# Performance work log

Hardware: AMD Instinct MI355X
Metric: run time of the kernel (lower is better)

The kernel has to match this reference:

```python
import jax, jax.numpy as jnp
import numpy as np

T, N, F_IN, H, HEADS, R, E, L, C = 8, 20000, 128, 128, 4, 12, 40000, 2, 16
D = H // HEADS


def setup_inputs() -> dict:
    key = jax.random.key(0)
    ks = jax.random.split(key, 24)
    s = 0.05  # weight scale to keep activations well-conditioned
    return {
        "x": jax.random.normal(ks[0], (T, N, F_IN), jnp.float32),
        "edge_src": jax.random.randint(ks[1], (R, E), 0, N),
        "edge_dst": jax.random.randint(ks[2], (R, E), 0, N),
        "rel_src_type": jax.random.randint(ks[3], (R,), 0, T),
        "rel_dst_type": jax.random.randint(ks[4], (R,), 0, T),
        "Wenc": jax.random.normal(ks[5], (T, F_IN, H)) * s,
        "benc": jax.random.normal(ks[6], (T, H)) * s,
        "Wk": jax.random.normal(ks[7], (L, T, H, H)) * s,
        "bk": jax.random.normal(ks[8], (L, T, H)) * s,
        "Wq": jax.random.normal(ks[9], (L, T, H, H)) * s,
        "bq": jax.random.normal(ks[10], (L, T, H)) * s,
        "Wv": jax.random.normal(ks[11], (L, T, H, H)) * s,
        "bv": jax.random.normal(ks[12], (L, T, H)) * s,
        "Wa": jax.random.normal(ks[13], (L, T, H, H)) * s,
        "ba": jax.random.normal(ks[14], (L, T, H)) * s,
        "skip": jax.random.normal(ks[15], (L, T)),
        "a_rel": jax.random.normal(ks[16], (L, R, HEADS, D, D)) * s,
        "m_rel": jax.random.normal(ks[17], (L, R, HEADS, D, D)) * s,
        "p_rel": jnp.ones((L, R, HEADS), jnp.float32),
        "Wout": jax.random.normal(ks[18], (H, C)) * s,
        "bout": jax.random.normal(ks[19], (C,)) * s,
    }


def _hgt_layer(x, Wk, bk, Wq, bq, Wv, bv, Wa, ba, skip, a_rel, m_rel, p_rel,
               edge_src, edge_dst, src_t, dst_t):
    # x: [T, N, H]; per-type k/q/v projections
    k = (jnp.einsum('tnh,thg->tng', x, Wk) + bk[:, None, :]).reshape(T, N, HEADS, D)
    q = (jnp.einsum('tnh,thg->tng', x, Wq) + bq[:, None, :]).reshape(T, N, HEADS, D)
    v = (jnp.einsum('tnh,thg->tng', x, Wv) + bv[:, None, :]).reshape(T, N, HEADS, D)

    # per-relation transforms on the (smaller) node side, then gather per edge
    k_rel = jnp.einsum('rnhd,rhde->rnhe', k[src_t], a_rel)  # [R, N, HEADS, D]
    v_rel = jnp.einsum('rnhd,rhde->rnhe', v[src_t], m_rel)
    gsrc = edge_src[:, :, None, None]
    gdst = edge_dst[:, :, None, None]
    k_e = jnp.take_along_axis(k_rel, gsrc, axis=1)          # [R, E, HEADS, D]
    v_e = jnp.take_along_axis(v_rel, gsrc, axis=1)
    q_e = jnp.take_along_axis(q[dst_t], gdst, axis=1)

    score = (q_e * k_e).sum(-1) * p_rel[:, None, :] / np.sqrt(D)  # [R, E, HEADS]

    # softmax per (edge-type, destination node): segment id = r*N + dst
    seg = (jnp.arange(R)[:, None] * N + edge_dst).reshape(-1)     # [R*E]
    sc = score.reshape(R * E, HEADS)
    m = jax.lax.stop_gradient(jax.ops.segment_max(sc, seg, num_segments=R * N))
    a = jnp.exp(sc - m[seg])
    denom = jax.ops.segment_sum(a, seg, num_segments=R * N)
    alpha = a / denom[seg]                                        # [R*E, HEADS]

    msg = (v_e.reshape(R * E, HEADS, D) * alpha[:, :, None]).reshape(R * E, H)
    # group='sum' across relations into (dst_type, dst_node)
    agg_seg = (dst_t[:, None] * N + edge_dst).reshape(-1)
    agg = jax.ops.segment_sum(msg, agg_seg, num_segments=T * N).reshape(T, N, H)

    out = jnp.einsum('tnh,thg->tng', jax.nn.gelu(agg, approximate=False), Wa) + ba[:, None, :]
    beta = jax.nn.sigmoid(skip)[:, None, None]
    return beta * out + (1.0 - beta) * x


def reference(x, edge_src, edge_dst, rel_src_type, rel_dst_type, Wenc, benc,
              Wk, bk, Wq, bq, Wv, bv, Wa, ba, skip, a_rel, m_rel, p_rel,
              Wout, bout):
    # per-node-type Linear + ReLU encode
    h = jax.nn.relu(jnp.einsum('tnf,tfh->tnh', x, Wenc) + benc[:, None, :])
    for l in range(L):
        h = _hgt_layer(h, Wk[l], bk[l], Wq[l], bq[l], Wv[l], bv[l], Wa[l], ba[l],
                       skip[l], a_rel[l], m_rel[l], p_rel[l],
                       edge_src, edge_dst, rel_src_type, rel_dst_type)
    # final Linear on the 'book' node type (index 0)
    return h[0] @ Wout + bout
```

## Files before the change

### kernel.cpp

```cpp
#include <hip/hip_runtime.h>
#include <cstdint>
#include <cstddef>

#define TT 8
#define NN 20000
#define FIN 128
#define HH 128
#define NHEADS 4
#define DD 32
#define RR 12
#define EE 40000
#define LL 2
#define CC 16
#define RN (RR*NN)
#define RE (RR*EE)
#define TNH ((size_t)TT*NN*HH)

struct Job { const float* in; const float* w; const float* b; float* out; };
struct Jobs8  { Job j[8]; };
struct Jobs16 { Job j[16]; };

__global__ __launch_bounds__(256) void zero_kernel(float4* __restrict__ p, int n4) {
    int i = blockIdx.x * 256 + threadIdx.x;
    int stride = gridDim.x * 256;
    for (; i < n4; i += stride) p[i] = make_float4(0.f, 0.f, 0.f, 0.f);
}

__global__ __launch_bounds__(256) void hist_kernel(const int* __restrict__ edge_dst,
                                                   int* __restrict__ cnt) {
    int g = blockIdx.x * 256 + threadIdx.x;
    if (g < RE) {
        int r = g / EE;
        atomicAdd(&cnt[r * NN + edge_dst[g]], 1);
    }
}

__global__ __launch_bounds__(256) void scan_local(const int* __restrict__ in,
                                                  int* __restrict__ out,
                                                  int* __restrict__ bsum, int n) {
    __shared__ int sh[256];
    int t = threadIdx.x;
    int base = blockIdx.x * 1024 + t * 4;
    int v0 = (base + 0 < n) ? in[base + 0] : 0;
    int v1 = (base + 1 < n) ? in[base + 1] : 0;
    int v2 = (base + 2 < n) ? in[base + 2] : 0;
    int v3 = (base + 3 < n) ? in[base + 3] : 0;
    int s = v0 + v1 + v2 + v3;
    sh[t] = s;
    __syncthreads();
    for (int off = 1; off < 256; off <<= 1) {
        int tmp = (t >= off) ? sh[t - off] : 0;
        __syncthreads();
        sh[t] += tmp;
        __syncthreads();
    }
    int incl = sh[t];
    int e = incl - s;
    if (t == 255) bsum[blockIdx.x] = incl;
    if (base + 0 < n) out[base + 0] = e; e += v0;
    if (base + 1 < n) out[base + 1] = e; e += v1;
    if (base + 2 < n) out[base + 2] = e; e += v2;
    if (base + 3 < n) out[base + 3] = e;
}

__global__ __launch_bounds__(256) void scan_bsum(int* __restrict__ bsum, int nb) {
    __shared__ int sh[256];
    int t = threadIdx.x;
    int v = (t < nb) ? bsum[t] : 0;
    sh[t] = v;
    __syncthreads();
    for (int off = 1; off < 256; off <<= 1) {
        int tmp = (t >= off) ? sh[t - off] : 0;
        __syncthreads();
        sh[t] += tmp;
        __syncthreads();
    }
    if (t < nb) bsum[t] = sh[t] - v;
}

__global__ __launch_bounds__(256) void scan_add(int* __restrict__ ofs,
                                                int* __restrict__ cursor,
                                                const int* __restrict__ bsum, int n) {
    int i = blockIdx.x * 256 + threadIdx.x;
    if (i < n) {
        int v = ofs[i] + bsum[i >> 10];
        ofs[i] = v;
        cursor[i] = v;
    }
}

__global__ __launch_bounds__(256) void scatter_kernel(const int* __restrict__ edge_dst,
                                                      int* __restrict__ cursor,
                                                      int* __restrict__ eidx) {
    int g = blockIdx.x * 256 + threadIdx.x;
    if (g < RE) {
        int r = g / EE;
        int pos = atomicAdd(&cursor[r * NN + edge_dst[g]], 1);
        eidx[pos] = g;
    }
}

template<int ACT, typename JT>
__global__ __launch_bounds__(256) void gemm128(const JT jt,
                                               const float* __restrict__ skip_l) {
    __shared__ float lw[32][128];
    __shared__ float li[32][132];
    const Job jb = jt.j[blockIdx.y];
    const int tid = threadIdx.x;
    const int row0 = blockIdx.x * 128;
    const int col = (tid & 31) * 4;
    const int rbase = (tid >> 5) * 16;
    float4 acc[16];
    #pragma unroll
    for (int i = 0; i < 16; i++) acc[i] = make_float4(0.f, 0.f, 0.f, 0.f);
    const float4 bb = *(const float4*)(jb.b + col);

    for (int k0 = 0; k0 < 128; k0 += 32) {
        #pragma unroll
        for (int it = 0; it < 4; ++it) {
            int idx = tid + it * 256;
            int kk = idx >> 5;
            int c4 = (idx & 31) * 4;
            *(float4*)&lw[kk][c4] = *(const float4*)(jb.w + (k0 + kk) * 128 + c4);
        }
        #pragma unroll
        for (int p = 0; p < 4; ++p) {
            int rr = (tid >> 3) + p * 32;
            int kk4 = (tid & 7) * 4;
            int rg = row0 + rr; if (rg >= NN) rg = NN - 1;
            float4 v = *(const float4*)(jb.in + (size_t)rg * 128 + k0 + kk4);
            if (ACT == 2) {
                v.x = 0.5f * v.x * (1.f + erff(v.x * 0.70710678118654752f));
                v.y = 0.5f * v.y * (1.f + erff(v.y * 0.70710678118654752f));
                v.z = 0.5f * v.z * (1.f + erff(v.z * 0.70710678118654752f));
                v.w = 0.5f * v.w * (1.f + erff(v.w * 0.70710678118654752f));
            }
            li[kk4 + 0][rr] = v.x; li[kk4 + 1][rr] = v.y;
            li[kk4 + 2][rr] = v.z; li[kk4 + 3][rr] = v.w;
        }
        __syncthreads();
        #pragma unroll 4
        for (int kk = 0; kk < 32; kk++) {
            const float4 bv = *(const float4*)&lw[kk][col];
            #pragma unroll
            for (int i4 = 0; i4 < 4; i4++) {
                float4 a4 = *(const float4*)&li[kk][rbase + 4 * i4];
                float4& A0 = acc[4 * i4 + 0];
                float4& A1 = acc[4 * i4 + 1];
                float4& A2 = acc[4 * i4 + 2];
                float4& A3 = acc[4 * i4 + 3];
                A0.x += a4.x * bv.x; A0.y += a4.x * bv.y; A0.z += a4.x * bv.z; A0.w += a4.x * bv.w;
                A1.x += a4.y * bv.x; A1.y += a4.y * bv.y; A1.z += a4.y * bv.z; A1.w += a4.y * bv.w;
                A2.x += a4.z * bv.x; A2.y += a4.z * bv.y; A2.z += a4.z * bv.z; A2.w += a4.z * bv.w;
                A3.x += a4.w * bv.x; A3.y += a4.w * bv.y; A3.z += a4.w * bv.z; A3.w += a4.w * bv.w;
            }
        }
        __syncthreads();
    }
    float beta = 0.f;
    if (ACT == 2) beta = 1.f / (1.f + __expf(-skip_l[blockIdx.y]));
    #pragma unroll
    for (int i = 0; i < 16; i++) {
        int rg = row0 + rbase + i;
        if (rg < NN) {
            float4 o = acc[i];
            o.x += bb.x; o.y += bb.y; o.z += bb.z; o.w += bb.w;
            float* op = jb.out + (size_t)rg * 128 + col;
            if (ACT == 1) {
                o.x = fmaxf(o.x, 0.f); o.y = fmaxf(o.y, 0.f);
                o.z = fmaxf(o.z, 0.f); o.w = fmaxf(o.w, 0.f);
            }
            if (ACT == 2) {
                float4 hv = *(const float4*)op;
                o.x = beta * o.x + (1.f - beta) * hv.x;
                o.y = beta * o.y + (1.f - beta) * hv.y;
                o.z = beta * o.z + (1.f - beta) * hv.z;
                o.w = beta * o.w + (1.f - beta) * hv.w;
            }
            *(float4*)op = o;
        }
    }
}

__global__ __launch_bounds__(256) void score_kernel(
        const int* __restrict__ ofs, const int* __restrict__ cnt, const int* __restrict__ eidx,
        const int* __restrict__ edge_src,
        const int* __restrict__ rel_src, const int* __restrict__ rel_dst,
        const float* __restrict__ qb, const float* __restrict__ kb,
        const float* __restrict__ a_rel_l, const float* __restrict__ p_rel_l,
        float* __restrict__ alpha, float* __restrict__ mbuf, float* __restrict__ dbuf) {
    int grp = threadIdx.x >> 7;
    int lane = threadIdx.x & 127;
    int seg = blockIdx.x * 2 + grp;
    if (seg >= RN) return;
    int c = cnt[seg];
    if (c == 0) return;
    int r = seg / NN, n = seg - r * NN;
    int tsrc = rel_src[r], tdst = rel_dst[r];
    int hh = lane >> 5;
    int hsel = threadIdx.x & 32;

    float qv = qb[((size_t)tdst * NN + n) * HH + lane];
    const float* Arow = a_rel_l + (((size_t)r * NHEADS + hh) * DD + (lane & 31)) * DD;
    float qa = 0.f;
    #pragma unroll
    for (int e = 0; e < 32; e += 4) {
        float4 a4 = *(const float4*)(Arow + e);
        qa += __shfl(qv, hsel + e + 0) * a4.x;
        qa += __shfl(qv, hsel + e + 1) * a4.y;
        qa += __shfl(qv, hsel + e + 2) * a4.z;
        qa += __shfl(qv, hsel + e + 3) * a4.w;
    }
    float pscale = p_rel_l[r * NHEADS + hh] * 0.17677669529663687f;
    int base = ofs[seg];
    float m = -INFINITY, den = 0.f;
    for (int i = 0; i < c; i++) {
        int g = eidx[base + i];
        int src = edge_src[g];
        float kv = kb[((size_t)tsrc * NN + src) * HH + lane];
        float prod = qa * kv;
        prod += __shfl_xor(prod, 16);
        prod += __shfl_xor(prod, 8);
        prod += __shfl_xor(prod, 4);
        prod += __shfl_xor(prod, 2);
        prod += __shfl_xor(prod, 1);
        float sc = prod * pscale;
        float mn = fmaxf(m, sc);
        den = den * __expf(m - mn) + __expf(sc - mn);
        m = mn;
        if ((lane & 31) == 0) alpha[(size_t)g * NHEADS + hh] = sc;
    }
    if ((lane & 31) == 0) {
        mbuf[(size_t)seg * NHEADS + hh] = m;
        dbuf[(size_t)seg * NHEADS + hh] = den;
    }
}

__global__ __launch_bounds__(256) void aggregate_kernel(
        const int* __restrict__ ofs, const int* __restrict__ cnt, const int* __restrict__ eidx,
        const int* __restrict__ edge_src,
        const int* __restrict__ rel_src, const int* __restrict__ rel_dst,
        const float* __restrict__ vb, const float* __restrict__ m_rel_l,
        const float* __restrict__ alpha, const float* __restrict__ mbuf,
        const float* __restrict__ dbuf, float* __restrict__ agg) {
    int grp = threadIdx.x >> 7;
    int lane = threadIdx.x & 127;
    int seg = blockIdx.x * 2 + grp;
    if (seg >= RN) return;
    int c = cnt[seg];
    if (c == 0) return;
    int r = seg / NN, n = seg - r * NN;
    int tsrc = rel_src[r], tdst = rel_dst[r];
    int hh = lane >> 5;
    int hsel = threadIdx.x & 32;

    float m = mbuf[(size_t)seg * NHEADS + hh];
    float inv = 1.f / dbuf[(size_t)seg * NHEADS + hh];
    int base = ofs[seg];
    float o = 0.f;
    for (int i = 0; i < c; i++) {
        int g = eidx[base + i];
        int src = edge_src[g];
        float sc = alpha[(size_t)g * NHEADS + hh];
        float a = __expf(sc - m) * inv;
        o += a * vb[((size_t)tsrc * NN + src) * HH + lane];
    }
    const float* Mcol = m_rel_l + ((size_t)r * NHEADS + hh) * DD * DD + (lane & 31);
    float oe = 0.f;
    #pragma unroll 8
    for (int d = 0; d < 32; d++) {
        oe += __shfl(o, hsel + d) * Mcol[d * 32];
    }
    atomicAdd(&agg[((size_t)tdst * NN + n) * HH + lane], oe);
}

__global__ __launch_bounds__(256) void final_kernel(const float* __restrict__ h0,
        const float* __restrict__ Wout, const float* __restrict__ bout,
        float* __restrict__ out) {
    __shared__ float w[128 * 16];
    __shared__ float hs[16][132];
    for (int i = threadIdx.x; i < 128 * 16; i += 256) w[i] = Wout[i];
    int row0 = blockIdx.x * 16;
    for (int i = threadIdx.x; i < 16 * 128; i += 256) {
        int rr = i >> 7, kk = i & 127;
        int rg = row0 + rr; if (rg >= NN) rg = NN - 1;
        hs[rr][kk] = h0[(size_t)rg * 128 + kk];
    }
    __syncthreads();
    int rr = threadIdx.x >> 4, colc = threadIdx.x & 15;
    float s = bout[colc];
    #pragma unroll 8
    for (int k = 0; k < 128; k++) s += hs[rr][k] * w[k * 16 + colc];
    int rg = row0 + rr;
    if (rg < NN) out[(size_t)rg * 16 + colc] = s;
}

extern "C" void kernel_launch(void* const* d_in, const int* in_sizes, int n_in,
                              void* d_out, int out_size, void* d_ws, size_t ws_size,
                              hipStream_t stream) {
    const float* x        = (const float*)d_in[0];
    const int*   edge_src = (const int*)d_in[1];
    const int*   edge_dst = (const int*)d_in[2];
    const int*   rel_src  = (const int*)d_in[3];
    const int*   rel_dst  = (const int*)d_in[4];
    const float* Wenc     = (const float*)d_in[5];
    const float* benc     = (const float*)d_in[6];
    const float* Wk       = (const float*)d_in[7];
    const float* bk       = (const float*)d_in[8];
    const float* Wq       = (const float*)d_in[9];
    const float* bq       = (const float*)d_in[10];
    const float* Wv       = (const float*)d_in[11];
    const float* bv       = (const float*)d_in[12];
    const float* Wa       = (const float*)d_in[13];
    const float* ba       = (const float*)d_in[14];
    const float* skip     = (const float*)d_in[15];
    const float* a_rel    = (const float*)d_in[16];
    const float* m_rel    = (const float*)d_in[17];
    const float* p_rel    = (const float*)d_in[18];
    const float* Wout     = (const float*)d_in[19];
    const float* bout     = (const float*)d_in[20];
    float* out = (float*)d_out;
    float* wsf = (float*)d_ws;

    const size_t NEED_FLOATS = 3 * TNH + (size_t)RE * NHEADS + 2 * (size_t)RN * NHEADS
                             + 3 * (size_t)RN + (size_t)RE + 256;
    if (ws_size < NEED_FLOATS * sizeof(float)) {
        zero_kernel<<<313, 256, 0, stream>>>((float4*)out, out_size / 4);
        return;
    }
    float* h    = wsf;
    float* buf1 = h    + TNH;
    float* buf2 = buf1 + TNH;
    float* alpha = buf2 + TNH;
    float* mbuf  = alpha + (size_t)RE * NHEADS;
    float* dbuf  = mbuf + (size_t)RN * NHEADS;
    int* cnt    = (int*)(dbuf + (size_t)RN * NHEADS);
    int* ofs    = cnt + RN;
    int* cursor = ofs + RN;
    int* eidx   = cursor + RN;
    int* bsum   = eidx + RE;

    const size_t NH = (size_t)NN * HH;
    const int RB = (NN + 127) / 128;

    zero_kernel<<<235, 256, 0, stream>>>((float4*)cnt, RN / 4);
    hist_kernel<<<(RE + 255) / 256, 256, 0, stream>>>(edge_dst, cnt);
    int nb = (RN + 1023) / 1024;
    scan_local<<<nb, 256, 0, stream>>>(cnt, ofs, bsum, RN);
    scan_bsum<<<1, 256, 0, stream>>>(bsum, nb);
    scan_add<<<(RN + 255) / 256, 256, 0, stream>>>(ofs, cursor, bsum, RN);
    scatter_kernel<<<(RE + 255) / 256, 256, 0, stream>>>(edge_dst, cursor, eidx);

    {
        Jobs8 je;
        for (int t = 0; t < 8; t++)
            je.j[t] = { x + t * NH, Wenc + (size_t)t * 128 * 128, benc + t * 128, h + t * NH };
        gemm128<1, Jobs8><<<dim3(RB, 8), 256, 0, stream>>>(je, nullptr);
    }

    for (int l = 0; l < LL; l++) {
        Jobs16 jqk;
        for (int t = 0; t < 8; t++) {
            size_t wi = (size_t)(l * TT + t) * 128 * 128;
            size_t bi = (size_t)(l * TT + t) * 128;
            jqk.j[t]     = { h + t * NH, Wq + wi, bq + bi, buf1 + t * NH };
            jqk.j[8 + t] = { h + t * NH, Wk + wi, bk + bi, buf2 + t * NH };
        }
        gemm128<0, Jobs16><<<dim3(RB, 16), 256, 0, stream>>>(jqk, nullptr);

        score_kernel<<<RN / 2, 256, 0, stream>>>(ofs, cnt, eidx, edge_src,
                rel_src, rel_dst, buf1, buf2,
                a_rel + (size_t)l * RR * NHEADS * DD * DD,
                p_rel + (size_t)l * RR * NHEADS, alpha, mbuf, dbuf);

        Jobs8 jv;
        for (int t = 0; t < 8; t++) {
            size_t wi = (size_t)(l * TT + t) * 128 * 128;
            size_t bi = (size_t)(l * TT + t) * 128;
            jv.j[t] = { h + t * NH, Wv + wi, bv + bi, buf1 + t * NH };
        }
        gemm128<0, Jobs8><<<dim3(RB, 8), 256, 0, stream>>>(jv, nullptr);

        zero_kernel<<<2048, 256, 0, stream>>>((float4*)buf2, (int)(TNH / 4));
        aggregate_kernel<<<RN / 2, 256, 0, stream>>>(ofs, cnt, eidx, edge_src,
                rel_src, rel_dst, buf1,
                m_rel + (size_t)l * RR * NHEADS * DD * DD,
                alpha, mbuf, dbuf, buf2);

        Jobs8 jo;
        for (int t = 0; t < 8; t++) {
            size_t wi = (size_t)(l * TT + t) * 128 * 128;
            size_t bi = (size_t)(l * TT + t) * 128;
            jo.j[t] = { buf2 + t * NH, Wa + wi, ba + bi, h + t * NH };
        }
        gemm128<2, Jobs8><<<dim3(RB, 8), 256, 0, stream>>>(jo, skip + l * TT);
    }

    final_kernel<<<NN / 16, 256, 0, stream>>>(h, Wout, bout, out);
}
```

Baseline: 2.445 ms.

## Parallelize score and aggregate per edge with a separate softmax stats pass

Score and aggregate kernels now run one 128-thread group per edge instead of one per destination segment. The scatter step stores the source index and segment id in sorted edge order, and a new stats kernel computes the per-segment max and inverse denominator. This removes the serial per-segment loops, their load imbalance and the indirection through eidx. In exchange, the q·A_rel product and the M_rel transform are recomputed for every edge, and atomicAdds into agg go from one per segment to one per edge.

```diff
diff --git a/kernel.cpp b/kernel.cpp
--- a/kernel.cpp
+++ b/kernel.cpp
@@ -90,13 +90,17 @@
 }
 
 __global__ __launch_bounds__(256) void scatter_kernel(const int* __restrict__ edge_dst,
+                                                      const int* __restrict__ edge_src,
                                                       int* __restrict__ cursor,
-                                                      int* __restrict__ eidx) {
+                                                      int* __restrict__ pos_src,
+                                                      int* __restrict__ pos_seg) {
     int g = blockIdx.x * 256 + threadIdx.x;
     if (g < RE) {
         int r = g / EE;
-        int pos = atomicAdd(&cursor[r * NN + edge_dst[g]], 1);
-        eidx[pos] = g;
+        int seg = r * NN + edge_dst[g];
+        int pos = atomicAdd(&cursor[seg], 1);
+        pos_src[pos] = edge_src[g];
+        pos_seg[pos] = seg;
     }
 }
 
@@ -183,24 +187,24 @@
 }
 
 __global__ __launch_bounds__(256) void score_kernel(
-        const int* __restrict__ ofs, const int* __restrict__ cnt, const int* __restrict__ eidx,
-        const int* __restrict__ edge_src,
+        const int* __restrict__ pos_src, const int* __restrict__ pos_seg,
         const int* __restrict__ rel_src, const int* __restrict__ rel_dst,
         const float* __restrict__ qb, const float* __restrict__ kb,
         const float* __restrict__ a_rel_l, const float* __restrict__ p_rel_l,
-        float* __restrict__ alpha, float* __restrict__ mbuf, float* __restrict__ dbuf) {
+        float* __restrict__ alpha) {
     int grp = threadIdx.x >> 7;
     int lane = threadIdx.x & 127;
-    int seg = blockIdx.x * 2 + grp;
-    if (seg >= RN) return;
-    int c = cnt[seg];
-    if (c == 0) return;
+    int p = blockIdx.x * 2 + grp;
+    if (p >= RE) return;
+    int seg = pos_seg[p];
+    int src = pos_src[p];
     int r = seg / NN, n = seg - r * NN;
     int tsrc = rel_src[r], tdst = rel_dst[r];
     int hh = lane >> 5;
     int hsel = threadIdx.x & 32;
 
     float qv = qb[((size_t)tdst * NN + n) * HH + lane];
+    float kv = kb[((size_t)tsrc * NN + src) * HH + lane];
     const float* Arow = a_rel_l + (((size_t)r * NHEADS + hh) * DD + (lane & 31)) * DD;
     float qa = 0.f;
     #pragma unroll
@@ -211,60 +215,60 @@
         qa += __shfl(qv, hsel + e + 2) * a4.z;
         qa += __shfl(qv, hsel + e + 3) * a4.w;
     }
-    float pscale = p_rel_l[r * NHEADS + hh] * 0.17677669529663687f;
+    float prod = qa * kv;
+    prod += __shfl_xor(prod, 16);
+    prod += __shfl_xor(prod, 8);
+    prod += __shfl_xor(prod, 4);
+    prod += __shfl_xor(prod, 2);
+    prod += __shfl_xor(prod, 1);
+    if ((lane & 31) == 0) {
+        float sc = prod * p_rel_l[r * NHEADS + hh] * 0.17677669529663687f;
+        alpha[(size_t)p * NHEADS + hh] = sc;
+    }
+}
+
+__global__ __launch_bounds__(256) void stats_kernel(
+        const int* __restrict__ ofs, const int* __restrict__ cnt,
+        const float* __restrict__ alpha,
+        float* __restrict__ mbuf, float* __restrict__ dbuf) {
+    int idx = blockIdx.x * 256 + threadIdx.x;
+    if (idx >= RN * NHEADS) return;
+    int seg = idx >> 2, hh = idx & 3;
+    int c = cnt[seg];
+    if (c == 0) return;
     int base = ofs[seg];
-    float m = -INFINITY, den = 0.f;
-    for (int i = 0; i < c; i++) {
-        int g = eidx[base + i];
-        int src = edge_src[g];
-        float kv = kb[((size_t)tsrc * NN + src) * HH + lane];
-        float prod = qa * kv;
-        prod += __shfl_xor(prod, 16);
-        prod += __shfl_xor(prod, 8);
-        prod += __shfl_xor(prod, 4);
-        prod += __shfl_xor(prod, 2);
-        prod += __shfl_xor(prod, 1);
-        float sc = prod * pscale;
-        float mn = fmaxf(m, sc);
-        den = den * __expf(m - mn) + __expf(sc - mn);
-        m = mn;
-        if ((lane & 31) == 0) alpha[(size_t)g * NHEADS + hh] = sc;
-    }
-    if ((lane & 31) == 0) {
-        mbuf[(size_t)seg * NHEADS + hh] = m;
-        dbuf[(size_t)seg * NHEADS + hh] = den;
-    }
+    float m = -INFINITY;
+    for (int i = 0; i < c; i++)
+        m = fmaxf(m, alpha[(size_t)(base + i) * NHEADS + hh]);
+    float den = 0.f;
+    for (int i = 0; i < c; i++)
+        den += __expf(alpha[(size_t)(base + i) * NHEADS + hh] - m);
+    mbuf[idx] = m;
+    dbuf[idx] = 1.f / den;
 }
 
 __global__ __launch_bounds__(256) void aggregate_kernel(
-        const int* __restrict__ ofs, const int* __restrict__ cnt, const int* __restrict__ eidx,
-        const int* __restrict__ edge_src,
+        const int* __restrict__ pos_src, const int* __restrict__ pos_seg,
         const int* __restrict__ rel_src, const int* __restrict__ rel_dst,
         const float* __restrict__ vb, const float* __restrict__ m_rel_l,
         const float* __restrict__ alpha, const float* __restrict__ mbuf,
         const float* __restrict__ dbuf, float* __restrict__ agg) {
     int grp = threadIdx.x >> 7;
     int lane = threadIdx.x & 127;
-    int seg = blockIdx.x * 2 + grp;
-    if (seg >= RN) return;
-    int c = cnt[seg];
-    if (c == 0) return;
+    int p = blockIdx.x * 2 + grp;
+    if (p >= RE) return;
+    int seg = pos_seg[p];
+    int src = pos_src[p];
     int r = seg / NN, n = seg - r * NN;
     int tsrc = rel_src[r], tdst = rel_dst[r];
     int hh = lane >> 5;
     int hsel = threadIdx.x & 32;
 
+    float sc = alpha[(size_t)p * NHEADS + hh];
     float m = mbuf[(size_t)seg * NHEADS + hh];
-    float inv = 1.f / dbuf[(size_t)seg * NHEADS + hh];
-    int base = ofs[seg];
-    float o = 0.f;
-    for (int i = 0; i < c; i++) {
-        int g = eidx[base + i];
-        int src = edge_src[g];
-        float sc = alpha[(size_t)g * NHEADS + hh];
-        float a = __expf(sc - m) * inv;
-        o += a * vb[((size_t)tsrc * NN + src) * HH + lane];
-    }
+    float inv = dbuf[(size_t)seg * NHEADS + hh];
+    float a = __expf(sc - m) * inv;
+    float o = a * vb[((size_t)tsrc * NN + src) * HH + lane];
     const float* Mcol = m_rel_l + ((size_t)r * NHEADS + hh) * DD * DD + (lane & 31);
     float oe = 0.f;
     #pragma unroll 8
@@ -323,7 +327,7 @@
     float* wsf = (float*)d_ws;
 
     const size_t NEED_FLOATS = 3 * TNH + (size_t)RE * NHEADS + 2 * (size_t)RN * NHEADS
-                             + 3 * (size_t)RN + (size_t)RE + 256;
+                             + 3 * (size_t)RN + 2 * (size_t)RE + 256;
     if (ws_size < NEED_FLOATS * sizeof(float)) {
         zero_kernel<<<313, 256, 0, stream>>>((float4*)out, out_size / 4);
         return;
@@ -334,11 +338,12 @@
     float* alpha = buf2 + TNH;
     float* mbuf  = alpha + (size_t)RE * NHEADS;
     float* dbuf  = mbuf + (size_t)RN * NHEADS;
-    int* cnt    = (int*)(dbuf + (size_t)RN * NHEADS);
-    int* ofs    = cnt + RN;
-    int* cursor = ofs + RN;
-    int* eidx   = cursor + RN;
-    int* bsum   = eidx + RE;
+    int* cnt     = (int*)(dbuf + (size_t)RN * NHEADS);
+    int* ofs     = cnt + RN;
+    int* cursor  = ofs + RN;
+    int* pos_src = cursor + RN;
+    int* pos_seg = pos_src + RE;
+    int* bsum    = pos_seg + RE;
 
     const size_t NH = (size_t)NN * HH;
     const int RB = (NN + 127) / 128;
@@ -349,7 +354,8 @@
     scan_local<<<nb, 256, 0, stream>>>(cnt, ofs, bsum, RN);
     scan_bsum<<<1, 256, 0, stream>>>(bsum, nb);
     scan_add<<<(RN + 255) / 256, 256, 0, stream>>>(ofs, cursor, bsum, RN);
-    scatter_kernel<<<(RE + 255) / 256, 256, 0, stream>>>(edge_dst, cursor, eidx);
+    scatter_kernel<<<(RE + 255) / 256, 256, 0, stream>>>(edge_dst, edge_src,
+                                                         cursor, pos_src, pos_seg);
 
     {
         Jobs8 je;
@@ -368,10 +374,12 @@
         }
         gemm128<0, Jobs16><<<dim3(RB, 16), 256, 0, stream>>>(jqk, nullptr);
 
-        score_kernel<<<RN / 2, 256, 0, stream>>>(ofs, cnt, eidx, edge_src,
+        score_kernel<<<RE / 2, 256, 0, stream>>>(pos_src, pos_seg,
                 rel_src, rel_dst, buf1, buf2,
                 a_rel + (size_t)l * RR * NHEADS * DD * DD,
-                p_rel + (size_t)l * RR * NHEADS, alpha, mbuf, dbuf);
+                p_rel + (size_t)l * RR * NHEADS, alpha);
+
+        stats_kernel<<<(RN * NHEADS + 255) / 256, 256, 0, stream>>>(ofs, cnt, alpha, mbuf, dbuf);
 
         Jobs8 jv;
         for (int t = 0; t < 8; t++) {
@@ -382,7 +390,7 @@
         gemm128<0, Jobs8><<<dim3(RB, 8), 256, 0, stream>>>(jv, nullptr);
 
         zero_kernel<<<2048, 256, 0, stream>>>((float4*)buf2, (int)(TNH / 4));
-        aggregate_kernel<<<RN / 2, 256, 0, stream>>>(ofs, cnt, eidx, edge_src,
+        aggregate_kernel<<<RE / 2, 256, 0, stream>>>(pos_src, pos_seg,
                 rel_src, rel_dst, buf1,
                 m_rel + (size_t)l * RR * NHEADS * DD * DD,
                 alpha, mbuf, dbuf, buf2);
```

Measured after the change: 3.367 ms. 1.38x slower.
